# Kernel optimization log

Measured on AMD Instinct MI355X. Metric: run time of the kernel, lower is better.

## Reference

```python
import jax, jax.numpy as jnp
import numpy as np

E = 1024
H = 16
F = 4096
EPS = 1e-5


def layer_norm(x, gamma, beta):
    mu = jnp.mean(x, axis=-1, keepdims=True)
    var = jnp.var(x, axis=-1, keepdims=True)
    return (x - mu) * jax.lax.rsqrt(var + EPS) * gamma + beta


def setup_inputs() -> dict:
    key = jax.random.key(0)
    ks = jax.random.split(key, 12)
    s = lambda d: 1.0 / np.sqrt(d)
    x = jax.random.normal(ks[0], (2, 2048, E), dtype=jnp.float32)
    Wq = jax.random.uniform(ks[1], (E, E), minval=-s(E), maxval=s(E))
    bq = jnp.zeros((E,), jnp.float32)
    Wk = jax.random.uniform(ks[2], (E, E), minval=-s(E), maxval=s(E))
    bk = jnp.zeros((E,), jnp.float32)
    Wv = jax.random.uniform(ks[3], (E, E), minval=-s(E), maxval=s(E))
    bv = jnp.zeros((E,), jnp.float32)
    Wo = jax.random.uniform(ks[4], (E, E), minval=-s(E), maxval=s(E))
    bo = jnp.zeros((E,), jnp.float32)
    g1 = jnp.ones((E,), jnp.float32)
    b1 = jnp.zeros((E,), jnp.float32)
    W1 = jax.random.uniform(ks[5], (E, F), minval=-s(E), maxval=s(E))
    bf1 = jnp.zeros((F,), jnp.float32)
    W2 = jax.random.uniform(ks[6], (F, E), minval=-s(F), maxval=s(F))
    bf2 = jnp.zeros((E,), jnp.float32)
    g2 = jnp.ones((E,), jnp.float32)
    b2 = jnp.zeros((E,), jnp.float32)
    return dict(x=x, Wq=Wq, bq=bq, Wk=Wk, bk=bk, Wv=Wv, bv=bv, Wo=Wo, bo=bo,
                g1=g1, b1=b1, W1=W1, bf1=bf1, W2=W2, bf2=bf2, g2=g2, b2=b2)


def reference(x, Wq, bq, Wk, bk, Wv, bv, Wo, bo, g1, b1, W1, bf1, W2, bf2, g2, b2):
    B, L, _ = x.shape
    Dh = E // H
    q = (x @ Wq + bq).reshape(B, L, H, Dh).transpose(0, 2, 1, 3)  # b h l d
    k = (x @ Wk + bk).reshape(B, L, H, Dh).transpose(0, 2, 1, 3)  # computed but unused (faithful to source)
    v = (x @ Wv + bv).reshape(B, L, H, Dh).transpose(0, 2, 1, 3)
    # NOTE: source computes scores as Q @ V^T (not K), scaled, then softmax
    scores = jnp.einsum('bhqd,bhkd->bhqk', q, v) / jnp.sqrt(jnp.float32(Dh))
    att = jax.nn.softmax(scores, axis=-1)
    ctx = jnp.einsum('bhqk,bhkd->bhqd', att, v)
    ctx = ctx.transpose(0, 2, 1, 3).reshape(B, L, E)
    att_out = ctx @ Wo + bo
    post_att = layer_norm(x + att_out, g1, b1)
    ff = jax.nn.relu(post_att @ W1 + bf1) @ W2 + bf2
    return layer_norm(post_att + ff, g2, b2)
```

## Files before the change

kernel.cpp:

```cpp
#include <hip/hip_runtime.h>
#include <stdint.h>

typedef unsigned short u16;
typedef __attribute__((ext_vector_type(8))) short short8;
typedef __attribute__((ext_vector_type(4))) float f32x4;
typedef __attribute__((ext_vector_type(4))) unsigned short u16x4;

#define TOKENS 4096
#define E_DIM 1024
#define F_DIM 4096
#define SEQ 2048
#define NH 16
#define DH 64

__device__ __forceinline__ u16 f2b(float f) {
  union { float f; unsigned u; } v; v.f = f;
  unsigned r = v.u + 0x7fffu + ((v.u >> 16) & 1u);
  return (u16)(r >> 16);
}

__device__ __forceinline__ void gl2lds16(const u16* g, u16* l) {
  __builtin_amdgcn_global_load_lds(
      (const __attribute__((address_space(1))) unsigned int*)(size_t)(g),
      (__attribute__((address_space(3))) unsigned int*)(unsigned int)(size_t)(l),
      16, 0, 0);
}

__global__ __launch_bounds__(256)
void transpose_w(const float* __restrict__ W, u16* __restrict__ Wt, int K, int N) {
  __shared__ float tile[32][33];
  const int kb = blockIdx.x * 32, nb = blockIdx.y * 32;
  const int tx = threadIdx.x & 31, ty = threadIdx.x >> 5;
#pragma unroll
  for (int i = 0; i < 32; i += 8)
    tile[ty + i][tx] = W[(size_t)(kb + ty + i) * N + nb + tx];
  __syncthreads();
#pragma unroll
  for (int i = 0; i < 32; i += 8)
    Wt[(size_t)(nb + ty + i) * K + kb + tx] = f2b(tile[tx][ty + i]);
}

__global__ __launch_bounds__(256)
void f32_to_bf16(const float* __restrict__ in, u16* __restrict__ out) {
  const int i = blockIdx.x * 256 + threadIdx.x;
  f32x4 f = ((const f32x4*)in)[i];
  u16x4 u;
#pragma unroll
  for (int j = 0; j < 4; j++) u[j] = f2b(f[j]);
  ((u16x4*)out)[i] = u;
}

__global__ __launch_bounds__(256)
void transpose_v(const u16* __restrict__ vsrc, u16* __restrict__ vt) {
  __shared__ u16 tile[64][66];
  const int kb = blockIdx.x * 64;
  const int bh = blockIdx.y;
  const int b = bh >> 4, h = bh & 15;
  {
    const int d = threadIdx.x & 63, r = threadIdx.x >> 6;
#pragma unroll
    for (int i = 0; i < 64; i += 4)
      tile[r + i][d] = vsrc[(size_t)(b * SEQ + kb + r + i) * E_DIM + h * DH + d];
  }
  __syncthreads();
  {
    const int pos = threadIdx.x & 63;
    const int srck = (pos & 3) * 16 + (pos >> 2);
#pragma unroll
    for (int j = 0; j < 64; j += 4) {
      const int d = (threadIdx.x >> 6) + j;
      vt[(size_t)(bh * DH + d) * SEQ + kb + pos] = tile[srck][d];
    }
  }
}

template <int RELU, int OUTBF>
__global__ __launch_bounds__(256)
void gemm_bt(const u16* __restrict__ A, const u16* __restrict__ Bt,
             const float* __restrict__ bias, void* __restrict__ Cout,
             int M, int N, int K) {
  __shared__ __align__(16) u16 As[128 * 32];
  __shared__ __align__(16) u16 Bs[128 * 32];
  const int tid = threadIdx.x;
  const int lane = tid & 63, wave = tid >> 6;
  const int mBlk = blockIdx.y * 128, nBlk = blockIdx.x * 128;
  const int wm = (wave >> 1) * 64, wn = (wave & 1) * 64;
  const int l15 = lane & 15, g = lane >> 4;

  f32x4 acc[4][4] = {};
  const int srow = lane >> 2;
  const int scol = (lane & 3) * 8;

  const u16* Ab = A + (size_t)mBlk * K;
  const u16* Bb = Bt + (size_t)nBlk * K;

  for (int k0 = 0; k0 < K; k0 += 32) {
    __syncthreads();
    for (int c = wave; c < 8; c += 4) {
      const int r = c * 16 + srow;
      gl2lds16(Ab + (size_t)r * K + k0 + scol, As + c * 512 + lane * 8);
      gl2lds16(Bb + (size_t)r * K + k0 + scol, Bs + c * 512 + lane * 8);
    }
    __syncthreads();

    short8 af[4], bf[4];
#pragma unroll
    for (int i = 0; i < 4; i++)
      af[i] = *(const short8*)(As + (wm + i * 16 + l15) * 32 + g * 8);
#pragma unroll
    for (int i = 0; i < 4; i++)
      bf[i] = *(const short8*)(Bs + (wn + i * 16 + l15) * 32 + g * 8);
#pragma unroll
    for (int mi = 0; mi < 4; mi++)
#pragma unroll
      for (int ni = 0; ni < 4; ni++)
        acc[mi][ni] = __builtin_amdgcn_mfma_f32_16x16x32_bf16(af[mi], bf[ni],
                                                              acc[mi][ni], 0, 0, 0);
  }

  const int row0 = mBlk + wm + g * 4;
  const int col0 = nBlk + wn + l15;
#pragma unroll
  for (int ni = 0; ni < 4; ni++) {
    const int c = col0 + ni * 16;
    const float bv = bias[c];
#pragma unroll
    for (int mi = 0; mi < 4; mi++) {
#pragma unroll
      for (int r = 0; r < 4; r++) {
        float v = acc[mi][ni][r] + bv;
        if (RELU) v = fmaxf(v, 0.f);
        const size_t idx = (size_t)(row0 + mi * 16 + r) * N + c;
        if (OUTBF) ((u16*)Cout)[idx] = f2b(v);
        else       ((float*)Cout)[idx] = v;
      }
    }
  }
}

template <int RELU, int OUTBF>
__global__ __launch_bounds__(512)
void gemm256(const u16* __restrict__ A, const u16* __restrict__ Bt,
             const float* __restrict__ bias, void* __restrict__ Cout,
             int N, int K) {
  __shared__ __align__(16) u16 lds[3][2][8192];
  const int tid = threadIdx.x;
  const int lane = tid & 63, wave = tid >> 6;
  const int wm = wave >> 2, wn = wave & 3;
  const int l15 = lane & 15, g = lane >> 4;

  const int bid = blockIdx.x;
  const int xcd = bid & 7, idx = bid >> 3;
  const int mT = (xcd >> 2) * 8 + (idx >> 2);
  const int nT = (xcd & 3) * 4 + (idx & 3);
  const int mBlk = mT * 256, nBlk = nT * 256;

  const u16* Ab = A + (size_t)mBlk * K;
  const u16* Bb = Bt + (size_t)nBlk * K;

  const int sm = lane >> 2;
  const int sk = (lane & 3) * 8;
  const u16* sa0 = Ab + (size_t)(wave * 16 + sm) * K + sk;
  const u16* sa1 = Ab + (size_t)((8 + wave) * 16 + sm) * K + sk;
  const u16* sb0 = Bb + (size_t)(wave * 16 + sm) * K + sk;
  const u16* sb1 = Bb + (size_t)((8 + wave) * 16 + sm) * K + sk;

  f32x4 acc[8][4] = {};

  const int NT = K >> 5;

#define STAGE_A(buf, t)                                             \
  {                                                                 \
    gl2lds16(sa0 + (size_t)(t) * 32, &lds[buf][0][wave * 512 + lane * 8]);       \
    gl2lds16(sa1 + (size_t)(t) * 32, &lds[buf][0][(8 + wave) * 512 + lane * 8]); \
  }
#define STAGE_B(buf, t)                                             \
  {                                                                 \
    gl2lds16(sb0 + (size_t)(t) * 32, &lds[buf][1][wave * 512 + lane * 8]);       \
    gl2lds16(sb1 + (size_t)(t) * 32, &lds[buf][1][(8 + wave) * 512 + lane * 8]); \
  }

  STAGE_A(0, 0) STAGE_B(0, 0)
  STAGE_A(1, 1) STAGE_B(1, 1)
  asm volatile("s_waitcnt vmcnt(4)" ::: "memory");
  asm volatile("s_barrier" ::: "memory");

  int buf = 0, sbuf = 2;
  for (int t = 0; t < NT; ++t) {
    const u16* As_ = &lds[buf][0][wm * (8 * 512)];
    const u16* Bs_ = &lds[buf][1][wn * (4 * 512)];
    const int fo = l15 * 32 + g * 8;

    short8 af[4], bfr[4];
#pragma unroll
    for (int i = 0; i < 4; i++)
      af[i] = *(const short8*)(As_ + i * 512 + fo);
#pragma unroll
    for (int i = 0; i < 4; i++)
      bfr[i] = *(const short8*)(Bs_ + i * 512 + fo);
    if (t + 2 < NT) STAGE_A(sbuf, t + 2)
    asm volatile("s_barrier" ::: "memory");
    asm volatile("s_waitcnt lgkmcnt(0)" ::: "memory");
    __builtin_amdgcn_sched_barrier(0);
    __builtin_amdgcn_s_setprio(1);
#pragma unroll
    for (int mg = 0; mg < 4; mg++)
#pragma unroll
      for (int ng = 0; ng < 4; ng++)
        acc[mg][ng] = __builtin_amdgcn_mfma_f32_16x16x32_bf16(af[mg], bfr[ng],
                                                              acc[mg][ng], 0, 0, 0);
    __builtin_amdgcn_s_setprio(0);
    asm volatile("s_barrier" ::: "memory");

#pragma unroll
    for (int i = 0; i < 4; i++)
      af[i] = *(const short8*)(As_ + (4 + i) * 512 + fo);
    if (t + 2 < NT) STAGE_B(sbuf, t + 2)
    asm volatile("s_barrier" ::: "memory");
    asm volatile("s_waitcnt lgkmcnt(0)" ::: "memory");
    __builtin_amdgcn_sched_barrier(0);
    __builtin_amdgcn_s_setprio(1);
#pragma unroll
    for (int mg = 0; mg < 4; mg++)
#pragma unroll
      for (int ng = 0; ng < 4; ng++)
        acc[4 + mg][ng] = __builtin_amdgcn_mfma_f32_16x16x32_bf16(af[mg], bfr[ng],
                                                                  acc[4 + mg][ng], 0, 0, 0);
    __builtin_amdgcn_s_setprio(0);
    if (t + 2 < NT) asm volatile("s_waitcnt vmcnt(4)" ::: "memory");
    else            asm volatile("s_waitcnt vmcnt(0)" ::: "memory");
    asm volatile("s_barrier" ::: "memory");

    buf = (buf == 2) ? 0 : buf + 1;
    sbuf = (sbuf == 2) ? 0 : sbuf + 1;
  }
#undef STAGE_A
#undef STAGE_B

  const int row0 = mBlk + wm * 128 + g * 4;
  const int col0 = nBlk + wn * 64 + l15;
#pragma unroll
  for (int ng = 0; ng < 4; ng++) {
    const int c = col0 + ng * 16;
    const float bv = bias[c];
#pragma unroll
    for (int mg = 0; mg < 8; mg++) {
#pragma unroll
      for (int r = 0; r < 4; r++) {
        float v = acc[mg][ng][r] + bv;
        if (RELU) v = fmaxf(v, 0.f);
        const size_t o = (size_t)(row0 + mg * 16 + r) * N + c;
        if (OUTBF) ((u16*)Cout)[o] = f2b(v);
        else       ((float*)Cout)[o] = v;
      }
    }
  }
}

__global__ __launch_bounds__(256)
void gemm_bt_sk(const u16* __restrict__ A, const u16* __restrict__ Bt,
                const float* __restrict__ bias, float* __restrict__ Cout,
                int M, int N, int K) {
  __shared__ __align__(16) u16 As[128 * 32];
  __shared__ __align__(16) u16 Bs[128 * 32];
  const int tid = threadIdx.x;
  const int lane = tid & 63, wave = tid >> 6;
  const int mBlk = blockIdx.y * 128, nBlk = blockIdx.x * 128;
  const int kz = blockIdx.z;
  const int Kh = K >> 1;
  const int wm = (wave >> 1) * 64, wn = (wave & 1) * 64;
  const int l15 = lane & 15, g = lane >> 4;

  f32x4 acc[4][4] = {};
  const int srow = lane >> 2;
  const int scol = (lane & 3) * 8;

  const u16* Ab = A + (size_t)mBlk * K + (size_t)kz * Kh;
  const u16* Bb = Bt + (size_t)nBlk * K + (size_t)kz * Kh;

  for (int k0 = 0; k0 < Kh; k0 += 32) {
    __syncthreads();
    for (int c = wave; c < 8; c += 4) {
      const int r = c * 16 + srow;
      gl2lds16(Ab + (size_t)r * K + k0 + scol, As + c * 512 + lane * 8);
      gl2lds16(Bb + (size_t)r * K + k0 + scol, Bs + c * 512 + lane * 8);
    }
    __syncthreads();

    short8 af[4], bf[4];
#pragma unroll
    for (int i = 0; i < 4; i++)
      af[i] = *(const short8*)(As + (wm + i * 16 + l15) * 32 + g * 8);
#pragma unroll
    for (int i = 0; i < 4; i++)
      bf[i] = *(const short8*)(Bs + (wn + i * 16 + l15) * 32 + g * 8);
#pragma unroll
    for (int mi = 0; mi < 4; mi++)
#pragma unroll
      for (int ni = 0; ni < 4; ni++)
        acc[mi][ni] = __builtin_amdgcn_mfma_f32_16x16x32_bf16(af[mi], bf[ni],
                                                              acc[mi][ni], 0, 0, 0);
  }

  float* out = Cout + (size_t)kz * M * N;
  const int row0 = mBlk + wm + g * 4;
  const int col0 = nBlk + wn + l15;
#pragma unroll
  for (int ni = 0; ni < 4; ni++) {
    const int c = col0 + ni * 16;
    const float bv = (kz == 0) ? bias[c] : 0.f;
#pragma unroll
    for (int mi = 0; mi < 4; mi++) {
#pragma unroll
      for (int r = 0; r < 4; r++)
        out[(size_t)(row0 + mi * 16 + r) * N + c] = acc[mi][ni][r] + bv;
    }
  }
}

__global__ __launch_bounds__(256)
void gemm_qv64(const u16* __restrict__ A, const u16* __restrict__ Bqv,
               const float* __restrict__ bq, const float* __restrict__ bv,
               u16* __restrict__ qout, u16* __restrict__ vout, int K) {
  __shared__ __align__(16) u16 As[128 * 32];
  __shared__ __align__(16) u16 Bs[64 * 32];
  const int tid = threadIdx.x;
  const int lane = tid & 63, wave = tid >> 6;
  const int mBlk = blockIdx.y * 128, nBlk = blockIdx.x * 64;
  const int isQ = nBlk < 1024;
  const int ncol = isQ ? nBlk : nBlk - 1024;
  const float* bias = isQ ? bq : bv;
  u16* out = isQ ? qout : vout;
  const float oscale = isQ ? 0.125f * 1.44269504088896f : 1.0f;
  const int wm = (wave >> 1) * 64, wn = (wave & 1) * 32;
  const int l15 = lane & 15, g = lane >> 4;

  f32x4 acc[4][2] = {};
  const int srow = lane >> 2;
  const int scol = (lane & 3) * 8;

  const u16* Ab = A + (size_t)mBlk * K;
  const u16* Bb = Bqv + (size_t)nBlk * K;

  for (int k0 = 0; k0 < K; k0 += 32) {
    __syncthreads();
    for (int c = wave; c < 8; c += 4) {
      const int r = c * 16 + srow;
      gl2lds16(Ab + (size_t)r * K + k0 + scol, As + c * 512 + lane * 8);
    }
    gl2lds16(Bb + (size_t)(wave * 16 + srow) * K + k0 + scol, Bs + wave * 512 + lane * 8);
    __syncthreads();

    short8 af[4], bf[2];
#pragma unroll
    for (int i = 0; i < 4; i++)
      af[i] = *(const short8*)(As + (wm + i * 16 + l15) * 32 + g * 8);
#pragma unroll
    for (int i = 0; i < 2; i++)
      bf[i] = *(const short8*)(Bs + (wn + i * 16 + l15) * 32 + g * 8);
#pragma unroll
    for (int mi = 0; mi < 4; mi++)
#pragma unroll
      for (int ni = 0; ni < 2; ni++)
        acc[mi][ni] = __builtin_amdgcn_mfma_f32_16x16x32_bf16(af[mi], bf[ni],
                                                              acc[mi][ni], 0, 0, 0);
  }

  const int row0 = mBlk + wm + g * 4;
  const int col0 = ncol + wn + l15;
#pragma unroll
  for (int ni = 0; ni < 2; ni++) {
    const int c = col0 + ni * 16;
    const float bv_ = bias[c];
#pragma unroll
    for (int mi = 0; mi < 4; mi++) {
#pragma unroll
      for (int r = 0; r < 4; r++) {
        float v = (acc[mi][ni][r] + bv_) * oscale;
        out[(size_t)(row0 + mi * 16 + r) * E_DIM + c] = f2b(v);
      }
    }
  }
}

__global__ __launch_bounds__(256)
void attn_kernel(const u16* __restrict__ qb, const u16* __restrict__ vb,
                 const u16* __restrict__ vtb, u16* __restrict__ ctxb) {
  __shared__ __align__(16) u16 Vs[2][64 * 64];
  __shared__ __align__(16) u16 Vts[2][64 * 64];
  __shared__ __align__(16) u16 Pl[4][16 * 64];
  const int tid = threadIdx.x;
  const int lane = tid & 63;
  const int wave = tid >> 6;
  const int l15 = lane & 15;
  const int g = lane >> 4;
  const int qblk = blockIdx.x;
  const int bh = blockIdx.y;
  const int b = bh >> 4;
  const int h = bh & 15;
  const int qrow = qblk * 64 + wave * 16;

  short8 aq0, aq1;
  {
    const u16* qp = qb + ((size_t)(b * SEQ + qrow + l15)) * E_DIM + h * DH + g * 8;
    aq0 = *(const short8*)(qp);
    aq1 = *(const short8*)(qp + 32);
  }

  f32x4 o[4] = {};
  float lsum[4] = {};

  u16* myPl = Pl[wave];

  const int srow = tid >> 3;
  const int sch = tid & 7;
  const int r0 = srow, r1 = 32 + srow;
  const u16* pv0 = vb + ((size_t)(b * SEQ) + r0) * E_DIM + h * DH + ((sch ^ (r0 & 7)) * 8);
  const u16* pv1 = vb + ((size_t)(b * SEQ) + r1) * E_DIM + h * DH + ((sch ^ (r1 & 7)) * 8);
  const u16* pt0 = vtb + ((size_t)bh * DH + r0) * SEQ + ((sch ^ (r0 & 7)) * 8);
  const u16* pt1 = vtb + ((size_t)bh * DH + r1) * SEQ + ((sch ^ (r1 & 7)) * 8);

#define STAGE(buf)                                      \
  {                                                     \
    gl2lds16(pv0, Vs[buf] + tid * 8);                   \
    gl2lds16(pv1, Vs[buf] + 2048 + tid * 8);            \
    gl2lds16(pt0, Vts[buf] + tid * 8);                  \
    gl2lds16(pt1, Vts[buf] + 2048 + tid * 8);           \
    pv0 += 64 * E_DIM; pv1 += 64 * E_DIM;               \
    pt0 += 64; pt1 += 64;                               \
  }

  STAGE(0)
  int cur = 0;

  for (int kc = 0; kc < SEQ; kc += 64) {
    asm volatile("s_barrier" ::: "memory");
    if (kc + 64 < SEQ) {
      STAGE(cur ^ 1)
      asm volatile("s_waitcnt vmcnt(4)" ::: "memory");
    } else {
      asm volatile("s_waitcnt vmcnt(0)" ::: "memory");
    }
    asm volatile("s_barrier" ::: "memory");

    const u16* VsC = Vs[cur];
    const u16* VtsC = Vts[cur];

    f32x4 s[4];
#pragma unroll
    for (int nt = 0; nt < 4; nt++) {
      const int key = nt * 16 + l15;
      const u16* vr = VsC + key * 64;
      short8 b0 = *(const short8*)(vr + ((g ^ (key & 7)) * 8));
      short8 b1 = *(const short8*)(vr + (((4 + g) ^ (key & 7)) * 8));
      f32x4 z = {};
      z = __builtin_amdgcn_mfma_f32_16x16x32_bf16(aq0, b0, z, 0, 0, 0);
      z = __builtin_amdgcn_mfma_f32_16x16x32_bf16(aq1, b1, z, 0, 0, 0);
      s[nt] = z;
    }

#pragma unroll
    for (int r = 0; r < 4; r++) {
      const int row = g * 4 + r;
      union { float f; unsigned u; } p0, p1, p2, p3;
      p0.f = __builtin_amdgcn_exp2f(s[0][r]);
      p1.f = __builtin_amdgcn_exp2f(s[1][r]);
      p2.f = __builtin_amdgcn_exp2f(s[2][r]);
      p3.f = __builtin_amdgcn_exp2f(s[3][r]);
      union { unsigned u; float f; } t0, t1, t2, t3;
      t0.u = p0.u & 0xffff0000u;
      t1.u = p1.u & 0xffff0000u;
      t2.u = p2.u & 0xffff0000u;
      t3.u = p3.u & 0xffff0000u;
      lsum[r] += (t0.f + t1.f) + (t2.f + t3.f);
      uint2 pk;
      pk.x = __builtin_amdgcn_perm(p1.u, p0.u, 0x07060302u);
      pk.y = __builtin_amdgcn_perm(p3.u, p2.u, 0x07060302u);
      *(uint2*)(myPl + row * 64 + (((l15 >> 1) ^ (row & 7)) << 3) + ((l15 & 1) << 2)) = pk;
    }

#pragma unroll
    for (int ks = 0; ks < 2; ks++) {
      const int rp = l15;
      short8 ap = *(const short8*)(myPl + rp * 64 + (((ks * 4 + g) ^ (rp & 7)) << 3));
#pragma unroll
      for (int dt = 0; dt < 4; dt++) {
        const int d = dt * 16 + l15;
        short8 bv = *(const short8*)(VtsC + d * 64 + (((ks * 4 + g) ^ (d & 7)) * 8));
        o[dt] = __builtin_amdgcn_mfma_f32_16x16x32_bf16(ap, bv, o[dt], 0, 0, 0);
      }
    }
    cur ^= 1;
  }
#undef STAGE

#pragma unroll
  for (int r = 0; r < 4; r++) {
    float l = lsum[r];
    l += __shfl_xor(l, 1);
    l += __shfl_xor(l, 2);
    l += __shfl_xor(l, 4);
    l += __shfl_xor(l, 8);
    const float inv = 1.0f / l;
    size_t base = ((size_t)(b * SEQ + qrow + g * 4 + r)) * E_DIM + h * DH;
#pragma unroll
    for (int dt = 0; dt < 4; dt++)
      ctxb[base + dt * 16 + l15] = f2b(o[dt][r] * inv);
  }
}

__global__ __launch_bounds__(256)
void add_ln3(const float* __restrict__ X, const float* __restrict__ Y0,
             const float* __restrict__ Y1,
             const float* __restrict__ gam, const float* __restrict__ bet,
             float* __restrict__ out32, u16* __restrict__ out16) {
  const int row = blockIdx.x;
  const int tid = threadIdx.x;
  const size_t base = (size_t)row * E_DIM;
  float v[4];
  float s = 0.f, sq = 0.f;
#pragma unroll
  for (int i = 0; i < 4; i++) {
    const int c = tid + i * 256;
    float x = X[base + c] + Y0[base + c] + Y1[base + c];
    v[i] = x; s += x; sq += x * x;
  }
#pragma unroll
  for (int off = 32; off; off >>= 1) {
    s += __shfl_xor(s, off);
    sq += __shfl_xor(sq, off);
  }
  __shared__ float sh[8];
  const int wave = tid >> 6, lane = tid & 63;
  if (lane == 0) { sh[wave] = s; sh[4 + wave] = sq; }
  __syncthreads();
  s = sh[0] + sh[1] + sh[2] + sh[3];
  sq = sh[4] + sh[5] + sh[6] + sh[7];
  const float mean = s * (1.f / 1024.f);
  const float var = sq * (1.f / 1024.f) - mean * mean;
  const float rstd = rsqrtf(var + 1e-5f);
#pragma unroll
  for (int i = 0; i < 4; i++) {
    const int c = tid + i * 256;
    float y = (v[i] - mean) * rstd * gam[c] + bet[c];
    out32[base + c] = y;
    if (out16) out16[base + c] = f2b(y);
  }
}

extern "C" void kernel_launch(void* const* d_in, const int* in_sizes, int n_in,
                              void* d_out, int out_size, void* d_ws, size_t ws_size,
                              hipStream_t stream) {
  const float* x   = (const float*)d_in[0];
  const float* Wq  = (const float*)d_in[1];
  const float* bq  = (const float*)d_in[2];
  const float* Wv  = (const float*)d_in[5];
  const float* bv  = (const float*)d_in[6];
  const float* Wo  = (const float*)d_in[7];
  const float* bo  = (const float*)d_in[8];
  const float* g1  = (const float*)d_in[9];
  const float* b1  = (const float*)d_in[10];
  const float* W1  = (const float*)d_in[11];
  const float* bf1 = (const float*)d_in[12];
  const float* W2  = (const float*)d_in[13];
  const float* bf2 = (const float*)d_in[14];
  const float* g2  = (const float*)d_in[15];
  const float* b2  = (const float*)d_in[16];

  char* w = (char*)d_ws;
  const size_t MB = 1024ull * 1024ull;
  u16*   xb   = (u16*)(w + 0);
  u16*   h1   = (u16*)(w + 8 * MB);
  u16*   qb   = (u16*)(w + 8 * MB);
  u16*   vb   = (u16*)(w + 16 * MB);
  u16*   vtb  = (u16*)(w + 24 * MB);
  u16*   ctxb = (u16*)(w + 32 * MB);
  float* att0 = (float*)(w + 40 * MB);
  float* ff0  = (float*)(w + 40 * MB);
  float* pa   = (float*)(w + 72 * MB);
  u16*   pab  = (u16*)(w + 88 * MB);
  u16*   WqT  = (u16*)(w + 96 * MB);
  u16*   WvT  = (u16*)(w + 98 * MB);
  u16*   WoT  = (u16*)(w + 100 * MB);
  u16*   W1T  = (u16*)(w + 102 * MB);
  u16*   W2T  = (u16*)(w + 110 * MB);

  transpose_w<<<dim3(32, 32), 256, 0, stream>>>(Wq, WqT, 1024, 1024);
  transpose_w<<<dim3(32, 32), 256, 0, stream>>>(Wv, WvT, 1024, 1024);
  transpose_w<<<dim3(32, 32), 256, 0, stream>>>(Wo, WoT, 1024, 1024);
  transpose_w<<<dim3(32, 128), 256, 0, stream>>>(W1, W1T, 1024, 4096);
  transpose_w<<<dim3(128, 32), 256, 0, stream>>>(W2, W2T, 4096, 1024);
  f32_to_bf16<<<TOKENS * E_DIM / 4 / 256, 256, 0, stream>>>(x, xb);

  gemm_qv64<<<dim3(32, 32), 256, 0, stream>>>(xb, WqT, bq, bv, qb, vb, 1024);
  transpose_v<<<dim3(32, 32), 256, 0, stream>>>(vb, vtb);
  attn_kernel<<<dim3(32, 32), 256, 0, stream>>>(qb, vb, vtb, ctxb);
  gemm_bt_sk<<<dim3(8, 32, 2), 256, 0, stream>>>(ctxb, WoT, bo, att0, TOKENS, 1024, 1024);
  add_ln3<<<TOKENS, 256, 0, stream>>>(x, att0, att0 + (size_t)TOKENS * 1024, g1, b1, pa, pab);
  gemm256<1, 1><<<dim3(256), 512, 0, stream>>>(pab, W1T, bf1, h1, 4096, 1024);
  gemm_bt_sk<<<dim3(8, 32, 2), 256, 0, stream>>>(h1, W2T, bf2, ff0, TOKENS, 1024, 4096);
  add_ln3<<<TOKENS, 256, 0, stream>>>(pa, ff0, ff0 + (size_t)TOKENS * 1024, g2, b2, (float*)d_out, (u16*)nullptr);
}
```

Measured before the change: 380.4 us.

## Replace split-K GEMMs with triple-buffered 256x128 XCD-mapped kernel and fragment-major LDS staging

Replaces the simple two-sync split-K 128x128 GEMM used for the Wo and W2 projections with a 512-thread, 256x128-tile kernel. The new kernel triple-buffers LDS with async global-to-LDS loads, uses barrier and waitcnt pipelining plus setprio around the MFMAs, and maps blocks across XCDs for cache locality. It also changes the staging layout in all GEMMs so each 16-row fragment is stored fragment-major, letting LDS reads be a contiguous lane*8 offset. The goal is to hide load latency and cut LDS bank conflicts, at the cost of more LDS per block and fewer resident blocks.

New measurement: 390.0 us. 2.5% more time.

```diff
diff --git a/kernel.cpp b/kernel.cpp
--- a/kernel.cpp
+++ b/kernel.cpp
@@ -70,70 +70,6 @@
     for (int j = 0; j < 64; j += 4) {
       const int d = (threadIdx.x >> 6) + j;
       vt[(size_t)(bh * DH + d) * SEQ + kb + pos] = tile[srck][d];
-    }
-  }
-}
-
-template <int RELU, int OUTBF>
-__global__ __launch_bounds__(256)
-void gemm_bt(const u16* __restrict__ A, const u16* __restrict__ Bt,
-             const float* __restrict__ bias, void* __restrict__ Cout,
-             int M, int N, int K) {
-  __shared__ __align__(16) u16 As[128 * 32];
-  __shared__ __align__(16) u16 Bs[128 * 32];
-  const int tid = threadIdx.x;
-  const int lane = tid & 63, wave = tid >> 6;
-  const int mBlk = blockIdx.y * 128, nBlk = blockIdx.x * 128;
-  const int wm = (wave >> 1) * 64, wn = (wave & 1) * 64;
-  const int l15 = lane & 15, g = lane >> 4;
-
-  f32x4 acc[4][4] = {};
-  const int srow = lane >> 2;
-  const int scol = (lane & 3) * 8;
-
-  const u16* Ab = A + (size_t)mBlk * K;
-  const u16* Bb = Bt + (size_t)nBlk * K;
-
-  for (int k0 = 0; k0 < K; k0 += 32) {
-    __syncthreads();
-    for (int c = wave; c < 8; c += 4) {
-      const int r = c * 16 + srow;
-      gl2lds16(Ab + (size_t)r * K + k0 + scol, As + c * 512 + lane * 8);
-      gl2lds16(Bb + (size_t)r * K + k0 + scol, Bs + c * 512 + lane * 8);
-    }
-    __syncthreads();
-
-    short8 af[4], bf[4];
-#pragma unroll
-    for (int i = 0; i < 4; i++)
-      af[i] = *(const short8*)(As + (wm + i * 16 + l15) * 32 + g * 8);
-#pragma unroll
-    for (int i = 0; i < 4; i++)
-      bf[i] = *(const short8*)(Bs + (wn + i * 16 + l15) * 32 + g * 8);
-#pragma unroll
-    for (int mi = 0; mi < 4; mi++)
-#pragma unroll
-      for (int ni = 0; ni < 4; ni++)
-        acc[mi][ni] = __builtin_amdgcn_mfma_f32_16x16x32_bf16(af[mi], bf[ni],
-                                                              acc[mi][ni], 0, 0, 0);
-  }
-
-  const int row0 = mBlk + wm + g * 4;
-  const int col0 = nBlk + wn + l15;
-#pragma unroll
-  for (int ni = 0; ni < 4; ni++) {
-    const int c = col0 + ni * 16;
-    const float bv = bias[c];
-#pragma unroll
-    for (int mi = 0; mi < 4; mi++) {
-#pragma unroll
-      for (int r = 0; r < 4; r++) {
-        float v = acc[mi][ni][r] + bv;
-        if (RELU) v = fmaxf(v, 0.f);
-        const size_t idx = (size_t)(row0 + mi * 16 + r) * N + c;
-        if (OUTBF) ((u16*)Cout)[idx] = f2b(v);
-        else       ((float*)Cout)[idx] = v;
-      }
     }
   }
 }
@@ -158,12 +94,12 @@
   const u16* Ab = A + (size_t)mBlk * K;
   const u16* Bb = Bt + (size_t)nBlk * K;
 
-  const int sm = lane >> 2;
-  const int sk = (lane & 3) * 8;
-  const u16* sa0 = Ab + (size_t)(wave * 16 + sm) * K + sk;
-  const u16* sa1 = Ab + (size_t)((8 + wave) * 16 + sm) * K + sk;
-  const u16* sb0 = Bb + (size_t)(wave * 16 + sm) * K + sk;
-  const u16* sb1 = Bb + (size_t)((8 + wave) * 16 + sm) * K + sk;
+  const int fr = lane & 15;
+  const int fc = (lane >> 4) * 8;
+  const u16* sa0 = Ab + (size_t)(wave * 16 + fr) * K + fc;
+  const u16* sa1 = Ab + (size_t)((8 + wave) * 16 + fr) * K + fc;
+  const u16* sb0 = Bb + (size_t)(wave * 16 + fr) * K + fc;
+  const u16* sb1 = Bb + (size_t)((8 + wave) * 16 + fr) * K + fc;
 
   f32x4 acc[8][4] = {};
 
@@ -189,7 +125,7 @@
   for (int t = 0; t < NT; ++t) {
     const u16* As_ = &lds[buf][0][wm * (8 * 512)];
     const u16* Bs_ = &lds[buf][1][wn * (4 * 512)];
-    const int fo = l15 * 32 + g * 8;
+    const int fo = lane * 8;
 
     short8 af[4], bfr[4];
 #pragma unroll
@@ -257,54 +193,81 @@
   }
 }
 
-__global__ __launch_bounds__(256)
-void gemm_bt_sk(const u16* __restrict__ A, const u16* __restrict__ Bt,
-                const float* __restrict__ bias, float* __restrict__ Cout,
-                int M, int N, int K) {
-  __shared__ __align__(16) u16 As[128 * 32];
-  __shared__ __align__(16) u16 Bs[128 * 32];
+__global__ __launch_bounds__(512)
+void gemm_wide_sk(const u16* __restrict__ A, const u16* __restrict__ Bt,
+                  const float* __restrict__ bias, float* __restrict__ Cout,
+                  int N, int K) {
+  __shared__ __align__(16) u16 lds[3][12288];
   const int tid = threadIdx.x;
   const int lane = tid & 63, wave = tid >> 6;
-  const int mBlk = blockIdx.y * 128, nBlk = blockIdx.x * 128;
-  const int kz = blockIdx.z;
+  const int wm = wave >> 1, wn = wave & 1;
+  const int l15 = lane & 15, g = lane >> 4;
+
+  const int bid = blockIdx.x;
+  const int xcd = bid & 7, idx = bid >> 3;
+  const int kz = xcd & 1;
+  const int nT = ((xcd >> 1) & 1) * 4 + (idx & 3);
+  const int mT = (xcd >> 2) * 8 + (idx >> 2);
+  const int mBlk = mT * 256, nBlk = nT * 128;
   const int Kh = K >> 1;
-  const int wm = (wave >> 1) * 64, wn = (wave & 1) * 64;
-  const int l15 = lane & 15, g = lane >> 4;
-
-  f32x4 acc[4][4] = {};
-  const int srow = lane >> 2;
-  const int scol = (lane & 3) * 8;
 
   const u16* Ab = A + (size_t)mBlk * K + (size_t)kz * Kh;
   const u16* Bb = Bt + (size_t)nBlk * K + (size_t)kz * Kh;
 
-  for (int k0 = 0; k0 < Kh; k0 += 32) {
-    __syncthreads();
-    for (int c = wave; c < 8; c += 4) {
-      const int r = c * 16 + srow;
-      gl2lds16(Ab + (size_t)r * K + k0 + scol, As + c * 512 + lane * 8);
-      gl2lds16(Bb + (size_t)r * K + k0 + scol, Bs + c * 512 + lane * 8);
-    }
-    __syncthreads();
-
-    short8 af[4], bf[4];
+  const int fr = lane & 15;
+  const int fc = (lane >> 4) * 8;
+  const u16* sa0 = Ab + (size_t)(wave * 16 + fr) * K + fc;
+  const u16* sa1 = Ab + (size_t)((8 + wave) * 16 + fr) * K + fc;
+  const u16* sb0 = Bb + (size_t)(wave * 16 + fr) * K + fc;
+
+  f32x4 acc[4][4] = {};
+  const int NT = Kh >> 5;
+
+#define WSTAGE(buf, t)                                                         \
+  {                                                                            \
+    gl2lds16(sa0 + (size_t)(t) * 32, &lds[buf][wave * 512 + lane * 8]);        \
+    gl2lds16(sa1 + (size_t)(t) * 32, &lds[buf][(8 + wave) * 512 + lane * 8]);  \
+    gl2lds16(sb0 + (size_t)(t) * 32, &lds[buf][8192 + wave * 512 + lane * 8]); \
+  }
+
+  WSTAGE(0, 0)
+  WSTAGE(1, 1)
+  asm volatile("s_waitcnt vmcnt(3)" ::: "memory");
+  asm volatile("s_barrier" ::: "memory");
+
+  int buf = 0, sbuf = 2;
+  for (int t = 0; t < NT; ++t) {
+    const u16* As_ = &lds[buf][wm * (4 * 512)];
+    const u16* Bs_ = &lds[buf][8192 + wn * (4 * 512)];
+    short8 af[4], bfr[4];
 #pragma unroll
     for (int i = 0; i < 4; i++)
-      af[i] = *(const short8*)(As + (wm + i * 16 + l15) * 32 + g * 8);
+      af[i] = *(const short8*)(As_ + i * 512 + lane * 8);
 #pragma unroll
     for (int i = 0; i < 4; i++)
-      bf[i] = *(const short8*)(Bs + (wn + i * 16 + l15) * 32 + g * 8);
+      bfr[i] = *(const short8*)(Bs_ + i * 512 + lane * 8);
+    if (t + 2 < NT) WSTAGE(sbuf, t + 2)
+    asm volatile("s_waitcnt lgkmcnt(0)" ::: "memory");
+    __builtin_amdgcn_sched_barrier(0);
+    __builtin_amdgcn_s_setprio(1);
 #pragma unroll
     for (int mi = 0; mi < 4; mi++)
 #pragma unroll
       for (int ni = 0; ni < 4; ni++)
-        acc[mi][ni] = __builtin_amdgcn_mfma_f32_16x16x32_bf16(af[mi], bf[ni],
+        acc[mi][ni] = __builtin_amdgcn_mfma_f32_16x16x32_bf16(af[mi], bfr[ni],
                                                               acc[mi][ni], 0, 0, 0);
-  }
-
-  float* out = Cout + (size_t)kz * M * N;
-  const int row0 = mBlk + wm + g * 4;
-  const int col0 = nBlk + wn + l15;
+    __builtin_amdgcn_s_setprio(0);
+    if (t + 2 < NT) asm volatile("s_waitcnt vmcnt(3)" ::: "memory");
+    else            asm volatile("s_waitcnt vmcnt(0)" ::: "memory");
+    asm volatile("s_barrier" ::: "memory");
+    buf = (buf == 2) ? 0 : buf + 1;
+    sbuf = (sbuf == 2) ? 0 : sbuf + 1;
+  }
+#undef WSTAGE
+
+  float* out = Cout + (size_t)kz * TOKENS * N;
+  const int row0 = mBlk + wm * 64 + g * 4;
+  const int col0 = nBlk + wn * 64 + l15;
 #pragma unroll
   for (int ni = 0; ni < 4; ni++) {
     const int c = col0 + ni * 16;
@@ -336,28 +299,26 @@
   const int l15 = lane & 15, g = lane >> 4;
 
   f32x4 acc[4][2] = {};
-  const int srow = lane >> 2;
-  const int scol = (lane & 3) * 8;
+  const int fr = lane & 15;
+  const int fc = (lane >> 4) * 8;
 
   const u16* Ab = A + (size_t)mBlk * K;
   const u16* Bb = Bqv + (size_t)nBlk * K;
 
   for (int k0 = 0; k0 < K; k0 += 32) {
     __syncthreads();
-    for (int c = wave; c < 8; c += 4) {
-      const int r = c * 16 + srow;
-      gl2lds16(Ab + (size_t)r * K + k0 + scol, As + c * 512 + lane * 8);
-    }
-    gl2lds16(Bb + (size_t)(wave * 16 + srow) * K + k0 + scol, Bs + wave * 512 + lane * 8);
+    for (int c = wave; c < 8; c += 4)
+      gl2lds16(Ab + (size_t)(c * 16 + fr) * K + k0 + fc, As + c * 512 + lane * 8);
+    gl2lds16(Bb + (size_t)(wave * 16 + fr) * K + k0 + fc, Bs + wave * 512 + lane * 8);
     __syncthreads();
 
     short8 af[4], bf[2];
 #pragma unroll
     for (int i = 0; i < 4; i++)
-      af[i] = *(const short8*)(As + (wm + i * 16 + l15) * 32 + g * 8);
+      af[i] = *(const short8*)(As + ((wm >> 4) + i) * 512 + lane * 8);
 #pragma unroll
     for (int i = 0; i < 2; i++)
-      bf[i] = *(const short8*)(Bs + (wn + i * 16 + l15) * 32 + g * 8);
+      bf[i] = *(const short8*)(Bs + ((wn >> 4) + i) * 512 + lane * 8);
 #pragma unroll
     for (int mi = 0; mi < 4; mi++)
 #pragma unroll
@@ -595,9 +556,9 @@
   gemm_qv64<<<dim3(32, 32), 256, 0, stream>>>(xb, WqT, bq, bv, qb, vb, 1024);
   transpose_v<<<dim3(32, 32), 256, 0, stream>>>(vb, vtb);
   attn_kernel<<<dim3(32, 32), 256, 0, stream>>>(qb, vb, vtb, ctxb);
-  gemm_bt_sk<<<dim3(8, 32, 2), 256, 0, stream>>>(ctxb, WoT, bo, att0, TOKENS, 1024, 1024);
+  gemm_wide_sk<<<dim3(256), 512, 0, stream>>>(ctxb, WoT, bo, att0, 1024, 1024);
   add_ln3<<<TOKENS, 256, 0, stream>>>(x, att0, att0 + (size_t)TOKENS * 1024, g1, b1, pa, pab);
   gemm256<1, 1><<<dim3(256), 512, 0, stream>>>(pab, W1T, bf1, h1, 4096, 1024);
-  gemm_bt_sk<<<dim3(8, 32, 2), 256, 0, stream>>>(h1, W2T, bf2, ff0, TOKENS, 1024, 4096);
+  gemm_wide_sk<<<dim3(256), 512, 0, stream>>>(h1, W2T, bf2, ff0, 1024, 4096);
   add_ln3<<<TOKENS, 256, 0, stream>>>(pa, ff0, ff0 + (size_t)TOKENS * 1024, g2, b2, (float*)d_out, (u16*)nullptr);
 }
```
